# Kernel optimization log

Measured on AMD Instinct MI355X. Metric: run time of the kernel, lower is better.

The kernel has to match this reference:

```python
import jax, jax.numpy as jnp
import numpy as np

N_NODES = 50000
N_EDGES = 800000
IN_FEATS = 256
OUT_FEATS = 32
NUM_HEADS = 8
NUM_ETYPES = 5


def setup_inputs() -> dict:
    key = jax.random.key(0)
    k1, k2, k3, k4, k5, k6 = jax.random.split(key, 6)
    feat = jax.random.normal(k1, (N_NODES, IN_FEATS), dtype=jnp.float32)
    # xavier_normal-ish scale for fc weight [H*D, in]
    fc_w = jax.random.normal(k2, (NUM_HEADS * OUT_FEATS, IN_FEATS), dtype=jnp.float32) * 0.088
    edge_emb = jax.random.normal(k3, (NUM_ETYPES, NUM_HEADS), dtype=jnp.float32)
    e_feat = jax.random.randint(k4, (N_EDGES,), 0, NUM_ETYPES)
    src = jax.random.randint(k5, (N_EDGES,), 0, N_NODES)
    dst = jax.random.randint(k6, (N_EDGES,), 0, N_NODES)
    return {"feat": feat, "fc_w": fc_w, "edge_emb": edge_emb,
            "e_feat": e_feat, "src": src, "dst": dst}


def reference(feat, fc_w, edge_emb, e_feat, src, dst):
    N = feat.shape[0]
    H, D = NUM_HEADS, OUT_FEATS
    # fc: [N, in] @ [in, H*D] -> [N, H, D]
    feat_src = (feat @ fc_w.T).reshape(N, H, D)
    # per-edge, per-head logits from edge-type embedding: [E, H]
    e = edge_emb[e_feat]
    # edge_softmax: softmax over incoming edges of each dst node, per head
    m = jax.ops.segment_max(e, dst, num_segments=N)          # [N, H]
    ex = jnp.exp(e - m[dst])                                  # [E, H]
    denom = jax.ops.segment_sum(ex, dst, num_segments=N)     # [N, H]
    attn = ex / denom[dst]                                    # [E, H]
    # attn_sum: sum of attention weights arriving at each dst (== 1 w/o dropout)
    attn_sum = jax.ops.segment_sum(attn, dst, num_segments=N)  # [N, H]
    # weighted aggregation: sum_e attn_e * feat_src[src_e]
    msg = feat_src[src] * attn[:, :, None]                    # [E, H, D]
    agg = jax.ops.segment_sum(msg, dst, num_segments=N)      # [N, H, D]
    rst = agg / (attn_sum[:, :, None] + 1e-12)
    return rst, attn
```

## Files before the change

### kernel.cpp

```cpp
#include <hip/hip_runtime.h>

typedef unsigned short u16;
typedef unsigned int u32;
typedef __attribute__((ext_vector_type(8))) short bf16x8;
typedef __attribute__((ext_vector_type(4))) float f32x4;

#define NND 50000
#define NE 800000
#define NH 8
#define ND 32
#define NTY 5

__device__ inline u16 f2bf(float x){
  u32 u = __float_as_uint(x);
  return (u16)((u + 0x7FFFu + ((u >> 16) & 1u)) >> 16);
}

__global__ __launch_bounds__(512, 4) void gemm_k(const float* __restrict__ A,
                                                 const float* __restrict__ W,
                                                 u16* __restrict__ C, int M){
  __shared__ float As[128 * 64];
  __shared__ u16  Ws[256 * 64];
  const int tid  = threadIdx.x;
  const int m0   = blockIdx.x * 128;
  const int lane = tid & 63, wid = tid >> 6;
  const int wm = (wid >> 2) * 64, wn = (wid & 3) * 64;
  const int ml = lane & 15, quad = lane >> 4;

  f32x4 acc[4][4] = {};

  const int ra = tid >> 2, ca = (tid & 3) * 4;
  int rag = m0 + ra; if (rag >= M) rag = M - 1;
  const float* aRow = A + (size_t)rag * 256;
  const int rw = tid >> 1, hw = tid & 1;
  const float* wRow = W + (size_t)rw * 256;

  for (int k0 = 0; k0 < 256; k0 += 64){
    #pragma unroll
    for (int q = 0; q < 4; q++){
      float4 v = *(const float4*)(aRow + k0 + (ca + q) * 4);
      *(float4*)(As + ra * 64 + (((ca + q) ^ (ra & 15)) * 4)) = v;
    }
    #pragma unroll
    for (int q = 0; q < 4; q++){
      int ck = hw * 4 + q;
      float4 u0 = *(const float4*)(wRow + k0 + ck * 8);
      float4 u1 = *(const float4*)(wRow + k0 + ck * 8 + 4);
      ushort4 h0 = make_ushort4(f2bf(u0.x), f2bf(u0.y), f2bf(u0.z), f2bf(u0.w));
      ushort4 h1 = make_ushort4(f2bf(u1.x), f2bf(u1.y), f2bf(u1.z), f2bf(u1.w));
      int cp = ck ^ (rw & 7);
      *(ushort4*)(Ws + rw * 64 + cp * 8) = h0;
      *(ushort4*)(Ws + rw * 64 + cp * 8 + 4) = h1;
    }
    __syncthreads();
    #pragma unroll
    for (int kk = 0; kk < 64; kk += 32){
      bf16x8 af[4], wf[4];
      #pragma unroll
      for (int t = 0; t < 4; t++){
        int r = wm + t * 16 + ml;
        int c0 = (kk >> 2) + quad * 2;
        float4 x0 = *(const float4*)(As + r * 64 + (((c0    ) ^ (r & 15)) * 4));
        float4 x1 = *(const float4*)(As + r * 64 + (((c0 + 1) ^ (r & 15)) * 4));
        af[t] = (bf16x8){ (short)f2bf(x0.x), (short)f2bf(x0.y), (short)f2bf(x0.z), (short)f2bf(x0.w),
                          (short)f2bf(x1.x), (short)f2bf(x1.y), (short)f2bf(x1.z), (short)f2bf(x1.w) };
      }
      #pragma unroll
      for (int t = 0; t < 4; t++){
        int n = wn + t * 16 + ml;
        int c = (kk >> 3) + quad;
        wf[t] = *(const bf16x8*)(Ws + n * 64 + ((c ^ (n & 7)) * 8));
      }
      #pragma unroll
      for (int i = 0; i < 4; i++)
        #pragma unroll
        for (int j = 0; j < 4; j++)
          acc[i][j] = __builtin_amdgcn_mfma_f32_16x16x32_bf16(af[i], wf[j], acc[i][j], 0, 0, 0);
    }
    __syncthreads();
  }
  #pragma unroll
  for (int i = 0; i < 4; i++){
    #pragma unroll
    for (int rr = 0; rr < 4; rr++){
      int row = m0 + wm + i * 16 + quad * 4 + rr;
      if (row < M){
        u16* crow = C + (size_t)row * 256 + wn;
        #pragma unroll
        for (int j = 0; j < 4; j++)
          crow[j * 16 + ml] = f2bf(acc[i][j][rr]);
      }
    }
  }
}

__global__ __launch_bounds__(256) void count_k(const int* __restrict__ dst,
                                               int* __restrict__ deg,
                                               int* __restrict__ epos){
  int e = blockIdx.x * 256 + threadIdx.x;
  if (e < NE) epos[e] = atomicAdd(&deg[dst[e]], 1);
}

__global__ __launch_bounds__(256) void scan1_k(const int* __restrict__ deg,
                                               int* __restrict__ offs,
                                               int* __restrict__ bsum){
  __shared__ int lds[256];
  int b = blockIdx.x, tid = threadIdx.x;
  int base = b * 1024 + tid * 4;
  int d[4]; int tsum = 0;
  #pragma unroll
  for (int j = 0; j < 4; j++){
    int node = base + j;
    int v = (node < NND) ? deg[node] : 0;
    d[j] = tsum; tsum += v;
  }
  lds[tid] = tsum; __syncthreads();
  for (int off = 1; off < 256; off <<= 1){
    int v = (tid >= off) ? lds[tid - off] : 0;
    __syncthreads();
    lds[tid] += v;
    __syncthreads();
  }
  int excl = lds[tid] - tsum;
  #pragma unroll
  for (int j = 0; j < 4; j++)
    if (base + j < NND) offs[base + j] = excl + d[j];
  if (tid == 255) bsum[b] = lds[tid];
}

__global__ __launch_bounds__(64) void scan2_k(const int* __restrict__ bsum,
                                              int* __restrict__ bbase, int nb){
  __shared__ int l[64];
  int tid = threadIdx.x;
  int v = (tid < nb) ? bsum[tid] : 0;
  l[tid] = v; __syncthreads();
  for (int off = 1; off < 64; off <<= 1){
    int u = (tid >= off) ? l[tid - off] : 0;
    __syncthreads();
    l[tid] += u;
    __syncthreads();
  }
  bbase[tid] = l[tid] - v;
}

__global__ __launch_bounds__(256) void scatter_k(const int* __restrict__ dst,
                                                 const int* __restrict__ src,
                                                 const int* __restrict__ ef,
                                                 const int* __restrict__ epos,
                                                 const int* __restrict__ offs,
                                                 const int* __restrict__ bbase,
                                                 int* __restrict__ csr){
  int e = blockIdx.x * 256 + threadIdx.x;
  if (e >= NE) return;
  int d = dst[e];
  int pos = offs[d] + bbase[d >> 10] + epos[e];
  csr[pos] = src[e] | (ef[e] << 16);
}

__global__ __launch_bounds__(256) void nden_k(const int* __restrict__ csr,
                                              const int* __restrict__ offs,
                                              const int* __restrict__ bbase,
                                              const int* __restrict__ deg,
                                              const float* __restrict__ emb,
                                              float* __restrict__ rd){
  __shared__ float wl[40];
  int tid = threadIdx.x;
  if (tid < 40){
    int t = tid >> 3, h = tid & 7;
    float m = emb[h];
    for (int tt = 1; tt < NTY; ++tt) m = fmaxf(m, emb[tt * 8 + h]);
    wl[tid] = expf(emb[t * 8 + h] - m);
  }
  __syncthreads();
  int n = blockIdx.x * 256 + tid;
  if (n >= NND) return;
  int s = offs[n] + bbase[n >> 10];
  int dcnt = deg[n];
  float sum[8] = {0,0,0,0,0,0,0,0};
  for (int i = 0; i < dcnt; i++){
    int t = ((u32)csr[s + i]) >> 16;
    #pragma unroll
    for (int h = 0; h < 8; h++) sum[h] += wl[t * 8 + h];
  }
  #pragma unroll
  for (int h = 0; h < 8; h++)
    rd[(size_t)n * 8 + h] = (sum[h] > 0.f) ? (1.f / sum[h]) : 0.f;
}

__global__ __launch_bounds__(256) void attn_k(const int* __restrict__ dst,
                                              const int* __restrict__ ef,
                                              const float* __restrict__ rd,
                                              const float* __restrict__ emb,
                                              float* __restrict__ attn){
  __shared__ float wl[40];
  int tid = threadIdx.x;
  if (tid < 40){
    int t = tid >> 3, h = tid & 7;
    float m = emb[h];
    for (int tt = 1; tt < NTY; ++tt) m = fmaxf(m, emb[tt * 8 + h]);
    wl[tid] = expf(emb[t * 8 + h] - m);
  }
  __syncthreads();
  int e = blockIdx.x * 256 + tid;
  if (e >= NE) return;
  int d = dst[e], t = ef[e];
  float4 r0 = *(const float4*)(rd + (size_t)d * 8);
  float4 r1 = *(const float4*)(rd + (size_t)d * 8 + 4);
  const float* wr = wl + t * 8;
  *(float4*)(attn + (size_t)e * 8)     = make_float4(wr[0]*r0.x, wr[1]*r0.y, wr[2]*r0.z, wr[3]*r0.w);
  *(float4*)(attn + (size_t)e * 8 + 4) = make_float4(wr[4]*r1.x, wr[5]*r1.y, wr[6]*r1.z, wr[7]*r1.w);
}

__device__ inline void acc8(uint4 v, float wt, float* a){
  a[0] += wt * __uint_as_float(v.x << 16);
  a[1] += wt * __uint_as_float(v.x & 0xFFFF0000u);
  a[2] += wt * __uint_as_float(v.y << 16);
  a[3] += wt * __uint_as_float(v.y & 0xFFFF0000u);
  a[4] += wt * __uint_as_float(v.z << 16);
  a[5] += wt * __uint_as_float(v.z & 0xFFFF0000u);
  a[6] += wt * __uint_as_float(v.w << 16);
  a[7] += wt * __uint_as_float(v.w & 0xFFFF0000u);
}

__global__ __launch_bounds__(256) void agg_k(const u16* __restrict__ fsrc,
                                             const int* __restrict__ csr,
                                             const int* __restrict__ offs,
                                             const int* __restrict__ bbase,
                                             const int* __restrict__ deg,
                                             const float* __restrict__ emb,
                                             float* __restrict__ rst){
  __shared__ float wl[40];
  int tid = threadIdx.x;
  if (tid < 40){
    int t = tid >> 3, h = tid & 7;
    float m = emb[h];
    for (int tt = 1; tt < NTY; ++tt) m = fmaxf(m, emb[tt * 8 + h]);
    wl[tid] = expf(emb[t * 8 + h] - m);
  }
  __syncthreads();
  int node = blockIdx.x * 8 + (tid >> 5);
  int sl = tid & 31;
  int c = sl * 8;
  int h = sl >> 2;
  int s = offs[node] + bbase[node >> 10];
  int e = s + deg[node];
  float a[8] = {0,0,0,0,0,0,0,0};
  float ss = 0.f;
  int i = s;
  for (; i + 3 < e; i += 4){
    int p0 = csr[i], p1 = csr[i+1], p2 = csr[i+2], p3 = csr[i+3];
    uint4 v0 = *(const uint4*)(fsrc + (size_t)(p0 & 0xFFFF) * 256 + c);
    uint4 v1 = *(const uint4*)(fsrc + (size_t)(p1 & 0xFFFF) * 256 + c);
    uint4 v2 = *(const uint4*)(fsrc + (size_t)(p2 & 0xFFFF) * 256 + c);
    uint4 v3 = *(const uint4*)(fsrc + (size_t)(p3 & 0xFFFF) * 256 + c);
    float w0 = wl[(((u32)p0) >> 16) * 8 + h];
    float w1 = wl[(((u32)p1) >> 16) * 8 + h];
    float w2 = wl[(((u32)p2) >> 16) * 8 + h];
    float w3 = wl[(((u32)p3) >> 16) * 8 + h];
    acc8(v0, w0, a); acc8(v1, w1, a); acc8(v2, w2, a); acc8(v3, w3, a);
    ss += (w0 + w1) + (w2 + w3);
  }
  for (; i < e; i++){
    int p0 = csr[i];
    uint4 v0 = *(const uint4*)(fsrc + (size_t)(p0 & 0xFFFF) * 256 + c);
    float w0 = wl[(((u32)p0) >> 16) * 8 + h];
    acc8(v0, w0, a);
    ss += w0;
  }
  float inv = 1.0f / (ss + 1e-12f);
  float* orow = rst + (size_t)node * 256 + c;
  *(float4*)(orow)     = make_float4(a[0]*inv, a[1]*inv, a[2]*inv, a[3]*inv);
  *(float4*)(orow + 4) = make_float4(a[4]*inv, a[5]*inv, a[6]*inv, a[7]*inv);
}

extern "C" void kernel_launch(void* const* d_in, const int* in_sizes, int n_in,
                              void* d_out, int out_size, void* d_ws, size_t ws_size,
                              hipStream_t stream) {
  const float* feat = (const float*)d_in[0];
  const float* fcw  = (const float*)d_in[1];
  const float* emb  = (const float*)d_in[2];
  const int*   ef   = (const int*)d_in[3];
  const int*   src  = (const int*)d_in[4];
  const int*   dst  = (const int*)d_in[5];

  float* rst  = (float*)d_out;
  float* attn = (float*)d_out + (size_t)NND * NH * ND;

  char* ws = (char*)d_ws;
  size_t o = 0;
  u16* fsrc    = (u16*)(ws + o);   o += (size_t)NND * 256 * 2;
  int* csr     = (int*)(ws + o);   o += (size_t)NE * 4;
  int* epos    = (int*)(ws + o);   o += (size_t)NE * 4;
  int* offs    = (int*)(ws + o);   o += 200064;
  int* deg     = (int*)(ws + o);   o += 200064;
  float* rd    = (float*)(ws + o); o += (size_t)NND * NH * 4;
  int* bsum    = (int*)(ws + o);   o += 256;
  int* bbase   = (int*)(ws + o);   o += 256;

  hipMemsetAsync(deg, 0, (size_t)NND * 4, stream);

  gemm_k<<<391, 512, 0, stream>>>(feat, fcw, fsrc, NND);
  count_k<<<(NE + 255) / 256, 256, 0, stream>>>(dst, deg, epos);
  scan1_k<<<(NND + 1023) / 1024, 256, 0, stream>>>(deg, offs, bsum);
  scan2_k<<<1, 64, 0, stream>>>(bsum, bbase, (NND + 1023) / 1024);
  scatter_k<<<(NE + 255) / 256, 256, 0, stream>>>(dst, src, ef, epos, offs, bbase, csr);
  nden_k<<<(NND + 255) / 256, 256, 0, stream>>>(csr, offs, bbase, deg, emb, rd);
  attn_k<<<(NE + 255) / 256, 256, 0, stream>>>(dst, ef, rd, emb, attn);
  agg_k<<<NND / 8, 256, 0, stream>>>(fsrc, csr, offs, bbase, deg, emb, rst);
}
```

Baseline: 285.2 us.

## Fuse denominator into per-head aggregation kernel and drop separate nden pass

New measurement: 324.2 us. +13.6%, slower.

```diff
diff --git a/kernel.cpp b/kernel.cpp
--- a/kernel.cpp
+++ b/kernel.cpp
@@ -157,34 +157,67 @@
   csr[pos] = src[e] | (ef[e] << 16);
 }
 
-__global__ __launch_bounds__(256) void nden_k(const int* __restrict__ csr,
-                                              const int* __restrict__ offs,
-                                              const int* __restrict__ bbase,
-                                              const int* __restrict__ deg,
-                                              const float* __restrict__ emb,
-                                              float* __restrict__ rd){
-  __shared__ float wl[40];
-  int tid = threadIdx.x;
-  if (tid < 40){
-    int t = tid >> 3, h = tid & 7;
-    float m = emb[h];
-    for (int tt = 1; tt < NTY; ++tt) m = fmaxf(m, emb[tt * 8 + h]);
-    wl[tid] = expf(emb[t * 8 + h] - m);
-  }
-  __syncthreads();
-  int n = blockIdx.x * 256 + tid;
-  if (n >= NND) return;
-  int s = offs[n] + bbase[n >> 10];
-  int dcnt = deg[n];
-  float sum[8] = {0,0,0,0,0,0,0,0};
-  for (int i = 0; i < dcnt; i++){
-    int t = ((u32)csr[s + i]) >> 16;
-    #pragma unroll
-    for (int h = 0; h < 8; h++) sum[h] += wl[t * 8 + h];
-  }
-  #pragma unroll
-  for (int h = 0; h < 8; h++)
-    rd[(size_t)n * 8 + h] = (sum[h] > 0.f) ? (1.f / sum[h]) : 0.f;
+__global__ __launch_bounds__(256) void agg_k(const u16* __restrict__ fsrc,
+                                             const int* __restrict__ csr,
+                                             const int* __restrict__ offs,
+                                             const int* __restrict__ bbase,
+                                             const int* __restrict__ deg,
+                                             const float* __restrict__ emb,
+                                             float* __restrict__ rst,
+                                             float* __restrict__ rd){
+  const int h = blockIdx.x & 7;
+  float m = emb[h];
+  #pragma unroll
+  for (int t = 1; t < NTY; ++t) m = fmaxf(m, emb[t * 8 + h]);
+  const float w0 = __expf(emb[0 * 8 + h] - m);
+  const float w1 = __expf(emb[1 * 8 + h] - m);
+  const float w2 = __expf(emb[2 * 8 + h] - m);
+  const float w3 = __expf(emb[3 * 8 + h] - m);
+  const float w4 = __expf(emb[4 * 8 + h] - m);
+
+  const int tid  = threadIdx.x;
+  const int node = (blockIdx.x >> 3) * 16 + (tid >> 4);
+  const int sl   = tid & 15;
+  const u16* base = fsrc + h * 32 + sl * 2;
+
+  const int s = offs[node] + bbase[node >> 10];
+  const int e = s + deg[node];
+  float a0 = 0.f, a1 = 0.f, ss = 0.f;
+  int i = s;
+  for (; i + 3 < e; i += 4){
+    int p0 = csr[i], p1 = csr[i+1], p2 = csr[i+2], p3 = csr[i+3];
+    u32 v0 = *(const u32*)(base + (size_t)(p0 & 0xFFFF) * 256);
+    u32 v1 = *(const u32*)(base + (size_t)(p1 & 0xFFFF) * 256);
+    u32 v2 = *(const u32*)(base + (size_t)(p2 & 0xFFFF) * 256);
+    u32 v3 = *(const u32*)(base + (size_t)(p3 & 0xFFFF) * 256);
+    int t0 = ((u32)p0) >> 16, t1 = ((u32)p1) >> 16;
+    int t2 = ((u32)p2) >> 16, t3 = ((u32)p3) >> 16;
+    float q0 = t0 == 0 ? w0 : t0 == 1 ? w1 : t0 == 2 ? w2 : t0 == 3 ? w3 : w4;
+    float q1 = t1 == 0 ? w0 : t1 == 1 ? w1 : t1 == 2 ? w2 : t1 == 3 ? w3 : w4;
+    float q2 = t2 == 0 ? w0 : t2 == 1 ? w1 : t2 == 2 ? w2 : t2 == 3 ? w3 : w4;
+    float q3 = t3 == 0 ? w0 : t3 == 1 ? w1 : t3 == 2 ? w2 : t3 == 3 ? w3 : w4;
+    a0 += q0 * __uint_as_float(v0 << 16);
+    a1 += q0 * __uint_as_float(v0 & 0xFFFF0000u);
+    a0 += q1 * __uint_as_float(v1 << 16);
+    a1 += q1 * __uint_as_float(v1 & 0xFFFF0000u);
+    a0 += q2 * __uint_as_float(v2 << 16);
+    a1 += q2 * __uint_as_float(v2 & 0xFFFF0000u);
+    a0 += q3 * __uint_as_float(v3 << 16);
+    a1 += q3 * __uint_as_float(v3 & 0xFFFF0000u);
+    ss += (q0 + q1) + (q2 + q3);
+  }
+  for (; i < e; i++){
+    int p0 = csr[i];
+    u32 v0 = *(const u32*)(base + (size_t)(p0 & 0xFFFF) * 256);
+    int t0 = ((u32)p0) >> 16;
+    float q0 = t0 == 0 ? w0 : t0 == 1 ? w1 : t0 == 2 ? w2 : t0 == 3 ? w3 : w4;
+    a0 += q0 * __uint_as_float(v0 << 16);
+    a1 += q0 * __uint_as_float(v0 & 0xFFFF0000u);
+    ss += q0;
+  }
+  float inv = 1.0f / (ss + 1e-12f);
+  *(float2*)(rst + (size_t)node * 256 + h * 32 + sl * 2) = make_float2(a0 * inv, a1 * inv);
+  if (sl == 0) rd[(size_t)node * 8 + h] = (ss > 0.f) ? (1.0f / ss) : 0.f;
 }
 
 __global__ __launch_bounds__(256) void attn_k(const int* __restrict__ dst,
@@ -198,7 +231,7 @@
     int t = tid >> 3, h = tid & 7;
     float m = emb[h];
     for (int tt = 1; tt < NTY; ++tt) m = fmaxf(m, emb[tt * 8 + h]);
-    wl[tid] = expf(emb[t * 8 + h] - m);
+    wl[tid] = __expf(emb[t * 8 + h] - m);
   }
   __syncthreads();
   int e = blockIdx.x * 256 + tid;
@@ -209,68 +242,6 @@
   const float* wr = wl + t * 8;
   *(float4*)(attn + (size_t)e * 8)     = make_float4(wr[0]*r0.x, wr[1]*r0.y, wr[2]*r0.z, wr[3]*r0.w);
   *(float4*)(attn + (size_t)e * 8 + 4) = make_float4(wr[4]*r1.x, wr[5]*r1.y, wr[6]*r1.z, wr[7]*r1.w);
-}
-
-__device__ inline void acc8(uint4 v, float wt, float* a){
-  a[0] += wt * __uint_as_float(v.x << 16);
-  a[1] += wt * __uint_as_float(v.x & 0xFFFF0000u);
-  a[2] += wt * __uint_as_float(v.y << 16);
-  a[3] += wt * __uint_as_float(v.y & 0xFFFF0000u);
-  a[4] += wt * __uint_as_float(v.z << 16);
-  a[5] += wt * __uint_as_float(v.z & 0xFFFF0000u);
-  a[6] += wt * __uint_as_float(v.w << 16);
-  a[7] += wt * __uint_as_float(v.w & 0xFFFF0000u);
-}
-
-__global__ __launch_bounds__(256) void agg_k(const u16* __restrict__ fsrc,
-                                             const int* __restrict__ csr,
-                                             const int* __restrict__ offs,
-                                             const int* __restrict__ bbase,
-                                             const int* __restrict__ deg,
-                                             const float* __restrict__ emb,
-                                             float* __restrict__ rst){
-  __shared__ float wl[40];
-  int tid = threadIdx.x;
-  if (tid < 40){
-    int t = tid >> 3, h = tid & 7;
-    float m = emb[h];
-    for (int tt = 1; tt < NTY; ++tt) m = fmaxf(m, emb[tt * 8 + h]);
-    wl[tid] = expf(emb[t * 8 + h] - m);
-  }
-  __syncthreads();
-  int node = blockIdx.x * 8 + (tid >> 5);
-  int sl = tid & 31;
-  int c = sl * 8;
-  int h = sl >> 2;
-  int s = offs[node] + bbase[node >> 10];
-  int e = s + deg[node];
-  float a[8] = {0,0,0,0,0,0,0,0};
-  float ss = 0.f;
-  int i = s;
-  for (; i + 3 < e; i += 4){
-    int p0 = csr[i], p1 = csr[i+1], p2 = csr[i+2], p3 = csr[i+3];
-    uint4 v0 = *(const uint4*)(fsrc + (size_t)(p0 & 0xFFFF) * 256 + c);
-    uint4 v1 = *(const uint4*)(fsrc + (size_t)(p1 & 0xFFFF) * 256 + c);
-    uint4 v2 = *(const uint4*)(fsrc + (size_t)(p2 & 0xFFFF) * 256 + c);
-    uint4 v3 = *(const uint4*)(fsrc + (size_t)(p3 & 0xFFFF) * 256 + c);
-    float w0 = wl[(((u32)p0) >> 16) * 8 + h];
-    float w1 = wl[(((u32)p1) >> 16) * 8 + h];
-    float w2 = wl[(((u32)p2) >> 16) * 8 + h];
-    float w3 = wl[(((u32)p3) >> 16) * 8 + h];
-    acc8(v0, w0, a); acc8(v1, w1, a); acc8(v2, w2, a); acc8(v3, w3, a);
-    ss += (w0 + w1) + (w2 + w3);
-  }
-  for (; i < e; i++){
-    int p0 = csr[i];
-    uint4 v0 = *(const uint4*)(fsrc + (size_t)(p0 & 0xFFFF) * 256 + c);
-    float w0 = wl[(((u32)p0) >> 16) * 8 + h];
-    acc8(v0, w0, a);
-    ss += w0;
-  }
-  float inv = 1.0f / (ss + 1e-12f);
-  float* orow = rst + (size_t)node * 256 + c;
-  *(float4*)(orow)     = make_float4(a[0]*inv, a[1]*inv, a[2]*inv, a[3]*inv);
-  *(float4*)(orow + 4) = make_float4(a[4]*inv, a[5]*inv, a[6]*inv, a[7]*inv);
 }
 
 extern "C" void kernel_launch(void* const* d_in, const int* in_sizes, int n_in,
@@ -304,7 +275,6 @@
   scan1_k<<<(NND + 1023) / 1024, 256, 0, stream>>>(deg, offs, bsum);
   scan2_k<<<1, 64, 0, stream>>>(bsum, bbase, (NND + 1023) / 1024);
   scatter_k<<<(NE + 255) / 256, 256, 0, stream>>>(dst, src, ef, epos, offs, bbase, csr);
-  nden_k<<<(NND + 255) / 256, 256, 0, stream>>>(csr, offs, bbase, deg, emb, rd);
+  agg_k<<<(NND / 16) * 8, 256, 0, stream>>>(fsrc, csr, offs, bbase, deg, emb, rst, rd);
   attn_k<<<(NE + 255) / 256, 256, 0, stream>>>(dst, ef, rd, emb, attn);
-  agg_k<<<NND / 8, 256, 0, stream>>>(fsrc, csr, offs, bbase, deg, emb, rst);
-}
+}
```
